# Kernel optimization log

Measured on AMD Instinct MI355X. Metric: run time of the kernel, lower is better.

The kernel has to match this reference:

```python
import jax, jax.numpy as jnp
from jax import lax
import numpy as np

# dims
B, C, H, W, T = 8, 2, 64, 64, 200
# per-layer neuron configs (defaults from NetworkBasic.__init__)
THETA = (30.0, 50.0, 100.0)
TAU_SR = (1.0, 2.0, 4.0)
TAU_REF = (1.0, 2.0, 4.0)
SCALE_REF = (1.0, 1.0, 1.0)
TAU_RHO = (1.0, 1.0, 10.0)


def psp(x, tau):
    """SLAYER synaptic response: first-order leaky integration over time axis (last).
    a[t] = exp(-1/tau) * a[t-1] + x[t]"""
    d = jnp.exp(jnp.asarray(-1.0 / tau, x.dtype))
    xt = jnp.moveaxis(x, -1, 0)  # [T, B, C, H, W]
    def step(a, xi):
        a = d * a + xi
        return a, a
    _, ys = lax.scan(step, jnp.zeros_like(xt[0]), xt)
    return jnp.moveaxis(ys, 0, -1)


def spike(u, theta, tau_ref, scale_ref, tau_rho):
    """SLAYER spiking unit: threshold + leaky refractory state, sequential over T.
    Forward emits hard spikes; surrogate (sigmoid) used only for gradients."""
    dref = jnp.exp(jnp.asarray(-1.0 / tau_ref, u.dtype))
    th = jnp.asarray(theta, u.dtype)
    ut = jnp.moveaxis(u, -1, 0)  # [T, ...]
    def step(r, ui):
        v = ui + r
        hard = (v >= th).astype(u.dtype)
        sur = jax.nn.sigmoid((v - th) / tau_rho)
        s = sur + lax.stop_gradient(hard - sur)  # straight-through surrogate
        r2 = dref * r - th * scale_ref * s       # refractory subtraction
        return r2, s
    _, s = lax.scan(step, jnp.zeros_like(ut[0]), ut)
    return jnp.moveaxis(s, 0, -1)


def conv2d_t(x, w, pad):
    """slayer.conv: spatial conv applied independently per timestep (kernel kxkx1, no bias)."""
    Bb, Cc, Hh, Ww, Tt = x.shape
    xt = jnp.moveaxis(x, -1, 1).reshape(Bb * Tt, Cc, Hh, Ww)
    y = lax.conv_general_dilated(xt, w, (1, 1), [(pad, pad), (pad, pad)],
                                 dimension_numbers=("NCHW", "OIHW", "NCHW"))
    O = w.shape[0]
    return jnp.moveaxis(y.reshape(Bb, Tt, O, Hh, Ww), 1, -1)


def convT2d_t(x, w):
    """slayer.convTranspose kernel=2 stride=2, per timestep (exact 2x upsample)."""
    Bb, Cc, Hh, Ww, Tt = x.shape
    xt = jnp.moveaxis(x, -1, 1).reshape(Bb * Tt, Cc, Hh, Ww)
    y = lax.conv_transpose(xt, w, (2, 2), "VALID",
                           dimension_numbers=("NCHW", "OIHW", "NCHW"))
    O = w.shape[0]
    return jnp.moveaxis(y.reshape(Bb, Tt, O, 2 * Hh, 2 * Ww), 1, -1)


def setup_inputs() -> dict:
    key = jax.random.key(0)
    k0, k1, k2, k3 = jax.random.split(key, 4)
    spikeInput = (jax.random.uniform(k0, (B, C, H, W, T)) < 0.3).astype(jnp.float32)
    w1 = jax.random.normal(k1, (8, 2, 5, 5), jnp.float32) * 10.0
    w2 = jax.random.normal(k2, (8, 8, 3, 3), jnp.float32) * 10.0
    wup = jax.random.normal(k3, (2, 8, 2, 2), jnp.float32) * 10.0
    return {"spikeInput": spikeInput, "w1": w1, "w2": w2, "wup": wup}


def reference(spikeInput, w1, w2, wup):
    Bb, Cc, Hh, Ww, Tt = spikeInput.shape
    psp1 = psp(spikeInput, TAU_SR[0])
    psp1_up = jax.image.resize(psp1, (Bb, Cc, 2 * Hh, 2 * Ww, Tt), method="linear")
    s1 = spike(conv2d_t(psp1, w1, 2), THETA[0], TAU_REF[0], SCALE_REF[0], TAU_RHO[0])
    s2 = spike(conv2d_t(psp(s1, TAU_SR[1]), w2, 1), THETA[1], TAU_REF[1], SCALE_REF[1], TAU_RHO[1])
    s3 = spike(convT2d_t(psp(s2, TAU_SR[2]), wup) + psp1_up,
               THETA[2], TAU_REF[2], SCALE_REF[2], TAU_RHO[2])
    return s3
```

## Files before the change

kernel.cpp:

```cpp
#include <hip/hip_runtime.h>

#define DEC1 0.36787944117144233f
#define DEC2 0.60653065971263342f
#define DEC3 0.77880078307140487f

typedef float v2f __attribute__((ext_vector_type(2)));

__global__ void prep_weights(const float* __restrict__ w1,
                             const float* __restrict__ w2,
                             const float* __restrict__ wup,
                             float* __restrict__ wr)
{
    int i = blockIdx.x * 256 + threadIdx.x;
    if (i < 400) {
        int o = i & 7, tap = i >> 3;
        int c = tap / 25, rem = tap % 25, ky = rem / 5, kx = rem % 5;
        wr[i] = w1[((o * 2 + c) * 5 + ky) * 5 + kx];
    }
    if (i < 576) {
        int o = i & 7, tap = i >> 3;
        int c = tap / 9, rem = tap % 9, ky = rem / 3, kx = rem % 3;
        wr[400 + i] = w2[((o * 8 + c) * 3 + ky) * 3 + kx];
    }
    if (i < 64) {
        int c = i & 7, r = i >> 3;
        int dj = r & 1, di = (r >> 1) & 1, o = r >> 2;
        wr[976 + i] = wup[((o * 8 + c) * 2 + (1 - di)) * 2 + (1 - dj)];
    }
}

static __device__ __forceinline__ float4 spike_psp4(float4 u, float th, float dref,
                                                    float dq, float& r, float& q)
{
    float4 qv; float v, s;
    v = __fadd_rn(u.x, r); s = (v >= th) ? 1.f : 0.f;
    r = __fsub_rn(__fmul_rn(dref, r), __fmul_rn(th, s));
    q = __fadd_rn(__fmul_rn(dq, q), s); qv.x = q;
    v = __fadd_rn(u.y, r); s = (v >= th) ? 1.f : 0.f;
    r = __fsub_rn(__fmul_rn(dref, r), __fmul_rn(th, s));
    q = __fadd_rn(__fmul_rn(dq, q), s); qv.y = q;
    v = __fadd_rn(u.z, r); s = (v >= th) ? 1.f : 0.f;
    r = __fsub_rn(__fmul_rn(dref, r), __fmul_rn(th, s));
    q = __fadd_rn(__fmul_rn(dq, q), s); qv.z = q;
    v = __fadd_rn(u.w, r); s = (v >= th) ? 1.f : 0.f;
    r = __fsub_rn(__fmul_rn(dref, r), __fmul_rn(th, s));
    q = __fadd_rn(__fmul_rn(dq, q), s); qv.w = q;
    return qv;
}

static __device__ __forceinline__ float4 spike4(float4 u, float th, float dref, float& r)
{
    float4 ov; float v, s;
    v = __fadd_rn(u.x, r); s = (v >= th) ? 1.f : 0.f;
    r = __fsub_rn(__fmul_rn(dref, r), __fmul_rn(th, s)); ov.x = s;
    v = __fadd_rn(u.y, r); s = (v >= th) ? 1.f : 0.f;
    r = __fsub_rn(__fmul_rn(dref, r), __fmul_rn(th, s)); ov.y = s;
    v = __fadd_rn(u.z, r); s = (v >= th) ? 1.f : 0.f;
    r = __fsub_rn(__fmul_rn(dref, r), __fmul_rn(th, s)); ov.z = s;
    v = __fadd_rn(u.w, r); s = (v >= th) ? 1.f : 0.f;
    r = __fsub_rn(__fmul_rn(dref, r), __fmul_rn(th, s)); ov.w = s;
    return ov;
}

#define PKFMA(ALO_, AHI_, WV_, DLO_, DHI_) { \
    v2f wv2_ = { (WV_), (WV_) }; \
    ALO_ = __builtin_elementwise_fma(wv2_, DLO_, ALO_); \
    AHI_ = __builtin_elementwise_fma(wv2_, DHI_, AHI_); }

#define PSP4(V_, X_, st) { \
    V_.x = __fadd_rn(__fmul_rn(DEC1, st),   X_.x); \
    V_.y = __fadd_rn(__fmul_rn(DEC1, V_.x), X_.y); \
    V_.z = __fadd_rn(__fmul_rn(DEC1, V_.y), X_.z); \
    V_.w = __fadd_rn(__fmul_rn(DEC1, V_.z), X_.w); st = V_.w; }

__global__ __launch_bounds__(256, 2)
void snn_fused(const float* __restrict__ spk,
               const float* __restrict__ wr,
               float* __restrict__ out)
{
    const int tid  = threadIdx.x;
    const int b    = blockIdx.x >> 6;
    const int tile = blockIdx.x & 63;
    const int gy0  = (tile >> 3) << 3;
    const int gx0  = (tile & 7) << 3;

    __shared__ float4 sP1[2][2][2][224];
    __shared__ float4 sP2[8][2][100];
    __shared__ float4 sP3[8][2][64];

    float aP0 = 0.f, aP1 = 0.f;
    float rB[4], qB[4];
    float rC[2] = {0.f, 0.f}, qC[2] = {0.f, 0.f};
    float r3[2] = {0.f, 0.f};
#pragma unroll
    for (int i = 0; i < 4; ++i) { rB[i] = 0.f; qB[i] = 0.f; }

    const int ary = tid / 14, arx = tid % 14;
    const int aidx = ary * 16 + arx;
    const int aiy = gy0 - 3 + ary, aix = gx0 - 3 + arx;
    const bool avalid = (tid < 196) && (aiy >= 0) && (aiy < 64) && (aix >= 0) && (aix < 64);
    const int aoff0 = avalid ? (((b * 2 + 0) * 64 + aiy) * 64 + aix) * 200 : 0;
    const int aoff1 = avalid ? (((b * 2 + 1) * 64 + aiy) * 64 + aix) * 200 : 0;

    const int bh   = __builtin_amdgcn_readfirstlane(tid >> 7);
    const int bpx  = tid & 127;
    int by_, bx_;
    if (bpx < 80) { by_ = bpx >> 3; bx_ = bpx & 7; }
    else          { int t2 = bpx - 80; by_ = t2 >> 1; bx_ = 8 + (t2 & 1); }
    const int by = by_, bx = bx_;
    const int bwr = by * 10 + bx;
    const int ochB = tid >> 7;

    const int ch2  = __builtin_amdgcn_readfirstlane(tid >> 7);
    const int cop  = __builtin_amdgcn_readfirstlane(tid >> 6) & 1;
    const int cpx  = tid & 63;
    const int cy   = cpx >> 3, cx = cpx & 7;
    const int och2 = (tid >> 6) * 2;

    const int od  = tid >> 7;
    const int ddi = (tid >> 6) & 1;
    const int dpx = tid & 63;
    const int dy  = dpx >> 3, dxx = dpx & 7;
    const int diy = gy0 + dy, dix = gx0 + dxx;

    const float ay  = ddi ? ((diy == 63) ? 1.f : 0.75f) : ((diy == 0) ? 0.f : 0.25f);
    const float byw = ddi ? ((diy == 63) ? 0.f : 0.25f) : ((diy == 0) ? 1.f : 0.75f);
    const float ax0 = (dix == 0)  ? 0.f : 0.25f;
    const float bx0 = (dix == 0)  ? 1.f : 0.75f;
    const float ax1 = (dix == 63) ? 1.f : 0.75f;
    const float bx1 = (dix == 63) ? 0.f : 0.25f;
    const int   didx = (dy + 2 + ddi) * 16 + (dxx + 2);

    float4 x00 = make_float4(0.f,0.f,0.f,0.f), x01 = x00, x10 = x00, x11 = x00;
    if (avalid) {
        x00 = *(const float4*)(spk + aoff0);
        x01 = *(const float4*)(spk + aoff0 + 4);
        x10 = *(const float4*)(spk + aoff1);
        x11 = *(const float4*)(spk + aoff1 + 4);
    }

#pragma unroll 1
    for (int ck = 0; ck < 25; ++ck) {
        const int t0 = ck * 8;
        const int p  = ck & 1;

        if (tid < 196) {
            float4 v;
            PSP4(v, x00, aP0); sP1[p][0][0][aidx] = v;
            PSP4(v, x01, aP0); sP1[p][0][1][aidx] = v;
            PSP4(v, x10, aP1); sP1[p][1][0][aidx] = v;
            PSP4(v, x11, aP1); sP1[p][1][1][aidx] = v;
            if (ck < 24 && avalid) {
                x00 = *(const float4*)(spk + aoff0 + t0 + 8);
                x01 = *(const float4*)(spk + aoff0 + t0 + 12);
                x10 = *(const float4*)(spk + aoff1 + t0 + 8);
                x11 = *(const float4*)(spk + aoff1 + t0 + 12);
            }
        }
        __syncthreads();

        if (bpx < 100) {
            v2f alo[8], ahi[8];
#pragma unroll
            for (int o = 0; o < 8; ++o) { alo[o] = (v2f)(0.f); ahi[o] = (v2f)(0.f); }
#pragma unroll 1
            for (int c = 0; c < 2; ++c) {
#pragma unroll 1
                for (int ky = 0; ky < 5; ++ky) {
                    const float4* r0 = &sP1[p][c][bh][(by + ky) * 16 + bx];
                    const float*  wrow = wr + (c * 25 + ky * 5) * 8;
#pragma unroll
                    for (int kx = 0; kx < 5; ++kx) {
                        float4 d = r0[kx];
                        v2f dlo = { d.x, d.y }, dhi = { d.z, d.w };
#pragma unroll
                        for (int o = 0; o < 8; ++o) {
                            float wv = wrow[kx * 8 + o];
                            PKFMA(alo[o], ahi[o], wv, dlo, dhi);
                        }
                    }
                }
            }
#pragma unroll
            for (int o = 0; o < 8; ++o)
                sP2[o][bh][bwr] = make_float4(alo[o].x, alo[o].y, ahi[o].x, ahi[o].y);
        }
        __syncthreads();

        if (bpx < 100) {
#pragma unroll
            for (int j = 0; j < 4; ++j) {
                const int o = ochB * 4 + j;
                float4 u0 = sP2[o][0][bwr];
                float4 u1 = sP2[o][1][bwr];
                float4 q0 = spike_psp4(u0, 30.f, DEC1, DEC2, rB[j], qB[j]);
                sP2[o][0][bwr] = q0;
                float4 q1 = spike_psp4(u1, 30.f, DEC1, DEC2, rB[j], qB[j]);
                sP2[o][1][bwr] = q1;
            }
        }
        __syncthreads();

        {
            v2f alo[4], ahi[4];
#pragma unroll
            for (int j = 0; j < 4; ++j) { alo[j] = (v2f)(0.f); ahi[j] = (v2f)(0.f); }
            const float* wC = wr + 400 + cop * 4;
#pragma unroll 1
            for (int c = 0; c < 8; ++c) {
#pragma unroll 1
                for (int ky = 0; ky < 3; ++ky) {
                    const float4* r0 = &sP2[c][ch2][(cy + ky) * 10 + cx];
                    const float*  wrow = wC + (c * 9 + ky * 3) * 8;
#pragma unroll
                    for (int kx = 0; kx < 3; ++kx) {
                        float4 d = r0[kx];
                        v2f dlo = { d.x, d.y }, dhi = { d.z, d.w };
#pragma unroll
                        for (int j = 0; j < 4; ++j) {
                            float wv = wrow[kx * 8 + j];
                            PKFMA(alo[j], ahi[j], wv, dlo, dhi);
                        }
                    }
                }
            }
#pragma unroll
            for (int j = 0; j < 4; ++j)
                sP3[cop * 4 + j][ch2][cpx] =
                    make_float4(alo[j].x, alo[j].y, ahi[j].x, ahi[j].y);
        }
        __syncthreads();

        {
#pragma unroll
            for (int j = 0; j < 2; ++j) {
                const int o = och2 + j;
                float4 u0 = sP3[o][0][cpx];
                float4 u1 = sP3[o][1][cpx];
                float4 q0 = spike_psp4(u0, 50.f, DEC2, DEC3, rC[j], qC[j]);
                sP3[o][0][cpx] = q0;
                float4 q1 = spike_psp4(u1, 50.f, DEC2, DEC3, rC[j], qC[j]);
                sP3[o][1][cpx] = q1;
            }
        }
        __syncthreads();

        {
#pragma unroll 1
            for (int h = 0; h < 2; ++h) {
                float4 p3[8];
#pragma unroll
                for (int c = 0; c < 8; ++c) p3[c] = sP3[c][h][dpx];
                float4 P0a = sP1[p][od][h][didx];
                float4 P0b = sP1[p][od][h][didx + 1];
                float4 P0c = sP1[p][od][h][didx + 2];
                float4 P1a = sP1[p][od][h][didx + 16];
                float4 P1b = sP1[p][od][h][didx + 17];
                float4 P1c = sP1[p][od][h][didx + 18];
#pragma unroll
                for (int dj = 0; dj < 2; ++dj) {
                    const float ax  = dj ? ax1 : ax0;
                    const float bxw = dj ? bx1 : bx0;
                    v2f tlo = (v2f)(0.f), thi = (v2f)(0.f);
                    const float* wD = wr + 976 + ((od * 2 + ddi) * 2 + dj) * 8;
#pragma unroll
                    for (int c = 0; c < 8; ++c) {
                        float wv = wD[c];
                        v2f dlo = { p3[c].x, p3[c].y }, dhi = { p3[c].z, p3[c].w };
                        PKFMA(tlo, thi, wv, dlo, dhi);
                    }
                    float4 tv = make_float4(tlo.x, tlo.y, thi.x, thi.y);
                    float4 A  = dj ? P0b : P0a;
                    float4 Bv = dj ? P0c : P0b;
                    float4 Cv = dj ? P1b : P1a;
                    float4 Dv = dj ? P1c : P1b;
                    float4 up, u; float ra, rb;
                    ra = __fadd_rn(__fmul_rn(ay, A.x),  __fmul_rn(byw, Cv.x));
                    rb = __fadd_rn(__fmul_rn(ay, Bv.x), __fmul_rn(byw, Dv.x));
                    up.x = __fadd_rn(__fmul_rn(ax, ra), __fmul_rn(bxw, rb));
                    ra = __fadd_rn(__fmul_rn(ay, A.y),  __fmul_rn(byw, Cv.y));
                    rb = __fadd_rn(__fmul_rn(ay, Bv.y), __fmul_rn(byw, Dv.y));
                    up.y = __fadd_rn(__fmul_rn(ax, ra), __fmul_rn(bxw, rb));
                    ra = __fadd_rn(__fmul_rn(ay, A.z),  __fmul_rn(byw, Cv.z));
                    rb = __fadd_rn(__fmul_rn(ay, Bv.z), __fmul_rn(byw, Dv.z));
                    up.z = __fadd_rn(__fmul_rn(ax, ra), __fmul_rn(bxw, rb));
                    ra = __fadd_rn(__fmul_rn(ay, A.w),  __fmul_rn(byw, Cv.w));
                    rb = __fadd_rn(__fmul_rn(ay, Bv.w), __fmul_rn(byw, Dv.w));
                    up.w = __fadd_rn(__fmul_rn(ax, ra), __fmul_rn(bxw, rb));
                    u.x = __fadd_rn(tv.x, up.x);
                    u.y = __fadd_rn(tv.y, up.y);
                    u.z = __fadd_rn(tv.z, up.z);
                    u.w = __fadd_rn(tv.w, up.w);
                    float4 ov = spike4(u, 100.f, DEC3, r3[dj]);
                    float* op = out + ((((b * 2 + od) * 128 + (2 * diy + ddi)) * 128)
                                       + (2 * dix + dj)) * 200 + t0 + h * 4;
                    *(float4*)op = ov;
                }
            }
        }
    }
}

extern "C" void kernel_launch(void* const* d_in, const int* in_sizes, int n_in,
                              void* d_out, int out_size, void* d_ws, size_t ws_size,
                              hipStream_t stream)
{
    const float* spk = (const float*)d_in[0];
    const float* w1  = (const float*)d_in[1];
    const float* w2  = (const float*)d_in[2];
    const float* wup = (const float*)d_in[3];
    float* outp = (float*)d_out;
    float* wr   = (float*)d_ws;

    prep_weights<<<dim3(3), dim3(256), 0, stream>>>(w1, w2, wup, wr);
    snn_fused<<<dim3(512), dim3(256), 0, stream>>>(spk, wr, outp);
}
```

Before: 569.6 us.

## Split block into producer/consumer halves pipelining layer-1 and layers 2-3 across chunks

The block is split into two 128-thread halves. The first half computes input PSP, conv1 and the layer-1 spike for chunk ck, while the second half runs conv2, the layer-2 spike, the transposed conv and the output spike for chunk ck-1. This cuts barriers per chunk from five to two and overlaps the two stage groups. In exchange each half does more work per thread, register pressure rises from more accumulators, and the loop gains one extra iteration to drain the pipeline.

```diff
diff --git a/kernel.cpp b/kernel.cpp
--- a/kernel.cpp
+++ b/kernel.cpp
@@ -88,89 +88,115 @@
     __shared__ float4 sP2[8][2][100];
     __shared__ float4 sP3[8][2][64];
 
-    float aP0 = 0.f, aP1 = 0.f;
-    float rB[4], qB[4];
-    float rC[2] = {0.f, 0.f}, qC[2] = {0.f, 0.f};
-    float r3[2] = {0.f, 0.f};
-#pragma unroll
-    for (int i = 0; i < 4; ++i) { rB[i] = 0.f; qB[i] = 0.f; }
-
-    const int ary = tid / 14, arx = tid % 14;
-    const int aidx = ary * 16 + arx;
-    const int aiy = gy0 - 3 + ary, aix = gx0 - 3 + arx;
-    const bool avalid = (tid < 196) && (aiy >= 0) && (aiy < 64) && (aix >= 0) && (aix < 64);
-    const int aoff0 = avalid ? (((b * 2 + 0) * 64 + aiy) * 64 + aix) * 200 : 0;
-    const int aoff1 = avalid ? (((b * 2 + 1) * 64 + aiy) * 64 + aix) * 200 : 0;
-
-    const int bh   = __builtin_amdgcn_readfirstlane(tid >> 7);
-    const int bpx  = tid & 127;
-    int by_, bx_;
-    if (bpx < 80) { by_ = bpx >> 3; bx_ = bpx & 7; }
-    else          { int t2 = bpx - 80; by_ = t2 >> 1; bx_ = 8 + (t2 & 1); }
-    const int by = by_, bx = bx_;
-    const int bwr = by * 10 + bx;
-    const int ochB = tid >> 7;
-
-    const int ch2  = __builtin_amdgcn_readfirstlane(tid >> 7);
-    const int cop  = __builtin_amdgcn_readfirstlane(tid >> 6) & 1;
-    const int cpx  = tid & 63;
-    const int cy   = cpx >> 3, cx = cpx & 7;
-    const int och2 = (tid >> 6) * 2;
-
-    const int od  = tid >> 7;
-    const int ddi = (tid >> 6) & 1;
-    const int dpx = tid & 63;
-    const int dy  = dpx >> 3, dxx = dpx & 7;
-    const int diy = gy0 + dy, dix = gx0 + dxx;
-
-    const float ay  = ddi ? ((diy == 63) ? 1.f : 0.75f) : ((diy == 0) ? 0.f : 0.25f);
-    const float byw = ddi ? ((diy == 63) ? 0.f : 0.25f) : ((diy == 0) ? 1.f : 0.75f);
-    const float ax0 = (dix == 0)  ? 0.f : 0.25f;
-    const float bx0 = (dix == 0)  ? 1.f : 0.75f;
-    const float ax1 = (dix == 63) ? 1.f : 0.75f;
-    const float bx1 = (dix == 63) ? 0.f : 0.25f;
-    const int   didx = (dy + 2 + ddi) * 16 + (dxx + 2);
+    const bool isP = tid < 128;
+
+    const bool u1ok = isP && ((tid + 128) < 196);
+    int aidx0 = 0, aoff00 = 0, aoff01 = 0; bool av0 = false;
+    int aidx1 = 0, aoff10 = 0, aoff11 = 0; bool av1 = false;
+    if (isP) {
+        int ry = tid / 14, rx = tid % 14;
+        aidx0 = ry * 16 + rx;
+        int iy = gy0 - 3 + ry, ix = gx0 - 3 + rx;
+        av0 = iy >= 0 && iy < 64 && ix >= 0 && ix < 64;
+        if (av0) { aoff00 = (((b*2+0)*64 + iy)*64 + ix)*200;
+                   aoff01 = (((b*2+1)*64 + iy)*64 + ix)*200; }
+        if (u1ok) {
+            int u = tid + 128; ry = u / 14; rx = u % 14;
+            aidx1 = ry * 16 + rx;
+            iy = gy0 - 3 + ry; ix = gx0 - 3 + rx;
+            av1 = iy >= 0 && iy < 64 && ix >= 0 && ix < 64;
+            if (av1) { aoff10 = (((b*2+0)*64 + iy)*64 + ix)*200;
+                       aoff11 = (((b*2+1)*64 + iy)*64 + ix)*200; }
+        }
+    }
+    float aP00 = 0.f, aP01 = 0.f, aP10 = 0.f, aP11 = 0.f;
+
+    int by = 0, bx = 0, bwr = 0;
+    { int bpx = tid;
+      if (bpx < 80) { by = bpx >> 3; bx = bpx & 7; }
+      else          { int t2 = bpx - 80; by = t2 >> 1; bx = 8 + (t2 & 1); }
+      bwr = by * 10 + bx; }
+    float rB[8], qB[8];
+#pragma unroll
+    for (int i = 0; i < 8; ++i) { rB[i] = 0.f; qB[i] = 0.f; }
+
+    const int qt  = tid & 127;
+    const int wq  = qt >> 6;
+    const int l   = qt & 63;
+    const int pxq = wq * 32 + (l & 31);
+    const int sel = l >> 5;
+    const int cy  = pxq >> 3, cx = pxq & 7;
+    const int diy = gy0 + cy, dix = gx0 + cx;
+    float rC[4], qC[4];
+#pragma unroll
+    for (int i = 0; i < 4; ++i) { rC[i] = 0.f; qC[i] = 0.f; }
+    float r3[2][2] = {{0.f, 0.f}, {0.f, 0.f}};
+    const float ay0  = (diy == 0)  ? 0.f : 0.25f, by0w = (diy == 0)  ? 1.f : 0.75f;
+    const float ay1  = (diy == 63) ? 1.f : 0.75f, by1w = (diy == 63) ? 0.f : 0.25f;
+    const float ax0  = (dix == 0)  ? 0.f : 0.25f, bx0w = (dix == 0)  ? 1.f : 0.75f;
+    const float ax1  = (dix == 63) ? 1.f : 0.75f, bx1w = (dix == 63) ? 0.f : 0.25f;
+    const int   didx0 = (cy + 2) * 16 + (cx + 2);
 
     float4 x00 = make_float4(0.f,0.f,0.f,0.f), x01 = x00, x10 = x00, x11 = x00;
-    if (avalid) {
-        x00 = *(const float4*)(spk + aoff0);
-        x01 = *(const float4*)(spk + aoff0 + 4);
-        x10 = *(const float4*)(spk + aoff1);
-        x11 = *(const float4*)(spk + aoff1 + 4);
-    }
-
-#pragma unroll 1
-    for (int ck = 0; ck < 25; ++ck) {
-        const int t0 = ck * 8;
-        const int p  = ck & 1;
-
-        if (tid < 196) {
-            float4 v;
-            PSP4(v, x00, aP0); sP1[p][0][0][aidx] = v;
-            PSP4(v, x01, aP0); sP1[p][0][1][aidx] = v;
-            PSP4(v, x10, aP1); sP1[p][1][0][aidx] = v;
-            PSP4(v, x11, aP1); sP1[p][1][1][aidx] = v;
-            if (ck < 24 && avalid) {
-                x00 = *(const float4*)(spk + aoff0 + t0 + 8);
-                x01 = *(const float4*)(spk + aoff0 + t0 + 12);
-                x10 = *(const float4*)(spk + aoff1 + t0 + 8);
-                x11 = *(const float4*)(spk + aoff1 + t0 + 12);
-            }
-        }
-        __syncthreads();
-
-        if (bpx < 100) {
+    float4 y00 = x00, y01 = x00, y10 = x00, y11 = x00;
+    if (av0) {
+        x00 = *(const float4*)(spk + aoff00);
+        x01 = *(const float4*)(spk + aoff00 + 4);
+        x10 = *(const float4*)(spk + aoff01);
+        x11 = *(const float4*)(spk + aoff01 + 4);
+    }
+    if (av1) {
+        y00 = *(const float4*)(spk + aoff10);
+        y01 = *(const float4*)(spk + aoff10 + 4);
+        y10 = *(const float4*)(spk + aoff11);
+        y11 = *(const float4*)(spk + aoff11 + 4);
+    }
+
+#pragma unroll 1
+    for (int ck = 0; ck < 26; ++ck) {
+        const int p = ck & 1;
+
+        if (isP) {
+            if (ck < 25) {
+                const int t0 = ck * 8;
+                float4 v;
+                PSP4(v, x00, aP00); sP1[p][0][0][aidx0] = v;
+                PSP4(v, x01, aP00); sP1[p][0][1][aidx0] = v;
+                PSP4(v, x10, aP01); sP1[p][1][0][aidx0] = v;
+                PSP4(v, x11, aP01); sP1[p][1][1][aidx0] = v;
+                if (u1ok) {
+                    PSP4(v, y00, aP10); sP1[p][0][0][aidx1] = v;
+                    PSP4(v, y01, aP10); sP1[p][0][1][aidx1] = v;
+                    PSP4(v, y10, aP11); sP1[p][1][0][aidx1] = v;
+                    PSP4(v, y11, aP11); sP1[p][1][1][aidx1] = v;
+                }
+                if (ck < 24) {
+                    if (av0) {
+                        x00 = *(const float4*)(spk + aoff00 + t0 + 8);
+                        x01 = *(const float4*)(spk + aoff00 + t0 + 12);
+                        x10 = *(const float4*)(spk + aoff01 + t0 + 8);
+                        x11 = *(const float4*)(spk + aoff01 + t0 + 12);
+                    }
+                    if (av1) {
+                        y00 = *(const float4*)(spk + aoff10 + t0 + 8);
+                        y01 = *(const float4*)(spk + aoff10 + t0 + 12);
+                        y10 = *(const float4*)(spk + aoff11 + t0 + 8);
+                        y11 = *(const float4*)(spk + aoff11 + t0 + 12);
+                    }
+                }
+            }
+        } else if (ck >= 1) {
             v2f alo[8], ahi[8];
 #pragma unroll
             for (int o = 0; o < 8; ++o) { alo[o] = (v2f)(0.f); ahi[o] = (v2f)(0.f); }
 #pragma unroll 1
-            for (int c = 0; c < 2; ++c) {
-#pragma unroll 1
-                for (int ky = 0; ky < 5; ++ky) {
-                    const float4* r0 = &sP1[p][c][bh][(by + ky) * 16 + bx];
-                    const float*  wrow = wr + (c * 25 + ky * 5) * 8;
-#pragma unroll
-                    for (int kx = 0; kx < 5; ++kx) {
+            for (int c = 0; c < 8; ++c) {
+#pragma unroll 1
+                for (int ky = 0; ky < 3; ++ky) {
+                    const float4* r0 = &sP2[c][sel][(cy + ky) * 10 + cx];
+                    const float*  wrow = wr + 400 + (c * 9 + ky * 3) * 8;
+#pragma unroll
+                    for (int kx = 0; kx < 3; ++kx) {
                         float4 d = r0[kx];
                         v2f dlo = { d.x, d.y }, dhi = { d.z, d.w };
 #pragma unroll
@@ -183,121 +209,125 @@
             }
 #pragma unroll
             for (int o = 0; o < 8; ++o)
-                sP2[o][bh][bwr] = make_float4(alo[o].x, alo[o].y, ahi[o].x, ahi[o].y);
+                sP3[o][sel][pxq] = make_float4(alo[o].x, alo[o].y, ahi[o].x, ahi[o].y);
         }
         __syncthreads();
 
-        if (bpx < 100) {
+        if (isP) {
+            if (ck < 25 && tid < 100) {
+                v2f a0lo[8], a0hi[8], a1lo[8], a1hi[8];
+#pragma unroll
+                for (int o = 0; o < 8; ++o) {
+                    a0lo[o] = (v2f)(0.f); a0hi[o] = (v2f)(0.f);
+                    a1lo[o] = (v2f)(0.f); a1hi[o] = (v2f)(0.f);
+                }
+#pragma unroll 1
+                for (int c = 0; c < 2; ++c) {
+#pragma unroll 1
+                    for (int ky = 0; ky < 5; ++ky) {
+                        const float4* r0 = &sP1[p][c][0][(by + ky) * 16 + bx];
+                        const float4* r1 = &sP1[p][c][1][(by + ky) * 16 + bx];
+                        const float*  wrow = wr + (c * 25 + ky * 5) * 8;
+#pragma unroll
+                        for (int kx = 0; kx < 5; ++kx) {
+                            float4 d0 = r0[kx], d1 = r1[kx];
+                            v2f d0lo = { d0.x, d0.y }, d0hi = { d0.z, d0.w };
+                            v2f d1lo = { d1.x, d1.y }, d1hi = { d1.z, d1.w };
+#pragma unroll
+                            for (int o = 0; o < 8; ++o) {
+                                float wv = wrow[kx * 8 + o];
+                                PKFMA(a0lo[o], a0hi[o], wv, d0lo, d0hi);
+                                PKFMA(a1lo[o], a1hi[o], wv, d1lo, d1hi);
+                            }
+                        }
+                    }
+                }
+#pragma unroll
+                for (int o = 0; o < 8; ++o) {
+                    float4 u0 = make_float4(a0lo[o].x, a0lo[o].y, a0hi[o].x, a0hi[o].y);
+                    float4 q0 = spike_psp4(u0, 30.f, DEC1, DEC2, rB[o], qB[o]);
+                    sP2[o][0][bwr] = q0;
+                    float4 u1 = make_float4(a1lo[o].x, a1lo[o].y, a1hi[o].x, a1hi[o].y);
+                    float4 q1 = spike_psp4(u1, 30.f, DEC1, DEC2, rB[o], qB[o]);
+                    sP2[o][1][bwr] = q1;
+                }
+            }
+        } else if (ck >= 1) {
+            const int pD  = (ck - 1) & 1;
+            const int t0m = (ck - 1) * 8;
 #pragma unroll
             for (int j = 0; j < 4; ++j) {
-                const int o = ochB * 4 + j;
-                float4 u0 = sP2[o][0][bwr];
-                float4 u1 = sP2[o][1][bwr];
-                float4 q0 = spike_psp4(u0, 30.f, DEC1, DEC2, rB[j], qB[j]);
-                sP2[o][0][bwr] = q0;
-                float4 q1 = spike_psp4(u1, 30.f, DEC1, DEC2, rB[j], qB[j]);
-                sP2[o][1][bwr] = q1;
+                const int o = sel * 4 + j;
+                float4 u0 = sP3[o][0][pxq];
+                float4 u1 = sP3[o][1][pxq];
+                float4 q0 = spike_psp4(u0, 50.f, DEC2, DEC3, rC[j], qC[j]);
+                sP3[o][0][pxq] = q0;
+                float4 q1 = spike_psp4(u1, 50.f, DEC2, DEC3, rC[j], qC[j]);
+                sP3[o][1][pxq] = q1;
+            }
+            float4 p30[8], p31[8];
+#pragma unroll
+            for (int c2 = 0; c2 < 8; ++c2) {
+                p30[c2] = sP3[c2][0][pxq];
+                p31[c2] = sP3[c2][1][pxq];
+            }
+#pragma unroll
+            for (int h = 0; h < 2; ++h) {
+#pragma unroll
+                for (int ddi = 0; ddi < 2; ++ddi) {
+                    const float ayv = ddi ? ay1 : ay0;
+                    const float byv = ddi ? by1w : by0w;
+                    const int base = didx0 + ddi * 16;
+                    float4 Pa = sP1[pD][sel][h][base];
+                    float4 Pb = sP1[pD][sel][h][base + 1];
+                    float4 Pc = sP1[pD][sel][h][base + 2];
+                    float4 Qa = sP1[pD][sel][h][base + 16];
+                    float4 Qb = sP1[pD][sel][h][base + 17];
+                    float4 Qc = sP1[pD][sel][h][base + 18];
+#pragma unroll
+                    for (int dj = 0; dj < 2; ++dj) {
+                        const float axv = dj ? ax1 : ax0;
+                        const float bxv = dj ? bx1w : bx0w;
+                        v2f tlo = (v2f)(0.f), thi = (v2f)(0.f);
+                        const float* wD = wr + 976 + ((sel * 2 + ddi) * 2 + dj) * 8;
+#pragma unroll
+                        for (int c2 = 0; c2 < 8; ++c2) {
+                            float wv = wD[c2];
+                            float4 pc = h ? p31[c2] : p30[c2];
+                            v2f dlo = { pc.x, pc.y }, dhi = { pc.z, pc.w };
+                            PKFMA(tlo, thi, wv, dlo, dhi);
+                        }
+                        float4 tv = make_float4(tlo.x, tlo.y, thi.x, thi.y);
+                        float4 A  = dj ? Pb : Pa;
+                        float4 Bv = dj ? Pc : Pb;
+                        float4 Cv = dj ? Qb : Qa;
+                        float4 Dv = dj ? Qc : Qb;
+                        float4 up, u; float ra, rb;
+                        ra = __fadd_rn(__fmul_rn(ayv, A.x),  __fmul_rn(byv, Cv.x));
+                        rb = __fadd_rn(__fmul_rn(ayv, Bv.x), __fmul_rn(byv, Dv.x));
+                        up.x = __fadd_rn(__fmul_rn(axv, ra), __fmul_rn(bxv, rb));
+                        ra = __fadd_rn(__fmul_rn(ayv, A.y),  __fmul_rn(byv, Cv.y));
+                        rb = __fadd_rn(__fmul_rn(ayv, Bv.y), __fmul_rn(byv, Dv.y));
+                        up.y = __fadd_rn(__fmul_rn(axv, ra), __fmul_rn(bxv, rb));
+                        ra = __fadd_rn(__fmul_rn(ayv, A.z),  __fmul_rn(byv, Cv.z));
+                        rb = __fadd_rn(__fmul_rn(ayv, Bv.z), __fmul_rn(byv, Dv.z));
+                        up.z = __fadd_rn(__fmul_rn(axv, ra), __fmul_rn(bxv, rb));
+                        ra = __fadd_rn(__fmul_rn(ayv, A.w),  __fmul_rn(byv, Cv.w));
+                        rb = __fadd_rn(__fmul_rn(ayv, Bv.w), __fmul_rn(byv, Dv.w));
+                        up.w = __fadd_rn(__fmul_rn(axv, ra), __fmul_rn(bxv, rb));
+                        u.x = __fadd_rn(tv.x, up.x);
+                        u.y = __fadd_rn(tv.y, up.y);
+                        u.z = __fadd_rn(tv.z, up.z);
+                        u.w = __fadd_rn(tv.w, up.w);
+                        float4 ov = spike4(u, 100.f, DEC3, r3[ddi][dj]);
+                        float* op = out + ((((b * 2 + sel) * 128 + (2 * diy + ddi)) * 128)
+                                           + (2 * dix + dj)) * 200 + t0m + h * 4;
+                        *(float4*)op = ov;
+                    }
+                }
             }
         }
         __syncthreads();
-
-        {
-            v2f alo[4], ahi[4];
-#pragma unroll
-            for (int j = 0; j < 4; ++j) { alo[j] = (v2f)(0.f); ahi[j] = (v2f)(0.f); }
-            const float* wC = wr + 400 + cop * 4;
-#pragma unroll 1
-            for (int c = 0; c < 8; ++c) {
-#pragma unroll 1
-                for (int ky = 0; ky < 3; ++ky) {
-                    const float4* r0 = &sP2[c][ch2][(cy + ky) * 10 + cx];
-                    const float*  wrow = wC + (c * 9 + ky * 3) * 8;
-#pragma unroll
-                    for (int kx = 0; kx < 3; ++kx) {
-                        float4 d = r0[kx];
-                        v2f dlo = { d.x, d.y }, dhi = { d.z, d.w };
-#pragma unroll
-                        for (int j = 0; j < 4; ++j) {
-                            float wv = wrow[kx * 8 + j];
-                            PKFMA(alo[j], ahi[j], wv, dlo, dhi);
-                        }
-                    }
-                }
-            }
-#pragma unroll
-            for (int j = 0; j < 4; ++j)
-                sP3[cop * 4 + j][ch2][cpx] =
-                    make_float4(alo[j].x, alo[j].y, ahi[j].x, ahi[j].y);
-        }
-        __syncthreads();
-
-        {
-#pragma unroll
-            for (int j = 0; j < 2; ++j) {
-                const int o = och2 + j;
-                float4 u0 = sP3[o][0][cpx];
-                float4 u1 = sP3[o][1][cpx];
-                float4 q0 = spike_psp4(u0, 50.f, DEC2, DEC3, rC[j], qC[j]);
-                sP3[o][0][cpx] = q0;
-                float4 q1 = spike_psp4(u1, 50.f, DEC2, DEC3, rC[j], qC[j]);
-                sP3[o][1][cpx] = q1;
-            }
-        }
-        __syncthreads();
-
-        {
-#pragma unroll 1
-            for (int h = 0; h < 2; ++h) {
-                float4 p3[8];
-#pragma unroll
-                for (int c = 0; c < 8; ++c) p3[c] = sP3[c][h][dpx];
-                float4 P0a = sP1[p][od][h][didx];
-                float4 P0b = sP1[p][od][h][didx + 1];
-                float4 P0c = sP1[p][od][h][didx + 2];
-                float4 P1a = sP1[p][od][h][didx + 16];
-                float4 P1b = sP1[p][od][h][didx + 17];
-                float4 P1c = sP1[p][od][h][didx + 18];
-#pragma unroll
-                for (int dj = 0; dj < 2; ++dj) {
-                    const float ax  = dj ? ax1 : ax0;
-                    const float bxw = dj ? bx1 : bx0;
-                    v2f tlo = (v2f)(0.f), thi = (v2f)(0.f);
-                    const float* wD = wr + 976 + ((od * 2 + ddi) * 2 + dj) * 8;
-#pragma unroll
-                    for (int c = 0; c < 8; ++c) {
-                        float wv = wD[c];
-                        v2f dlo = { p3[c].x, p3[c].y }, dhi = { p3[c].z, p3[c].w };
-                        PKFMA(tlo, thi, wv, dlo, dhi);
-                    }
-                    float4 tv = make_float4(tlo.x, tlo.y, thi.x, thi.y);
-                    float4 A  = dj ? P0b : P0a;
-                    float4 Bv = dj ? P0c : P0b;
-                    float4 Cv = dj ? P1b : P1a;
-                    float4 Dv = dj ? P1c : P1b;
-                    float4 up, u; float ra, rb;
-                    ra = __fadd_rn(__fmul_rn(ay, A.x),  __fmul_rn(byw, Cv.x));
-                    rb = __fadd_rn(__fmul_rn(ay, Bv.x), __fmul_rn(byw, Dv.x));
-                    up.x = __fadd_rn(__fmul_rn(ax, ra), __fmul_rn(bxw, rb));
-                    ra = __fadd_rn(__fmul_rn(ay, A.y),  __fmul_rn(byw, Cv.y));
-                    rb = __fadd_rn(__fmul_rn(ay, Bv.y), __fmul_rn(byw, Dv.y));
-                    up.y = __fadd_rn(__fmul_rn(ax, ra), __fmul_rn(bxw, rb));
-                    ra = __fadd_rn(__fmul_rn(ay, A.z),  __fmul_rn(byw, Cv.z));
-                    rb = __fadd_rn(__fmul_rn(ay, Bv.z), __fmul_rn(byw, Dv.z));
-                    up.z = __fadd_rn(__fmul_rn(ax, ra), __fmul_rn(bxw, rb));
-                    ra = __fadd_rn(__fmul_rn(ay, A.w),  __fmul_rn(byw, Cv.w));
-                    rb = __fadd_rn(__fmul_rn(ay, Bv.w), __fmul_rn(byw, Dv.w));
-                    up.w = __fadd_rn(__fmul_rn(ax, ra), __fmul_rn(bxw, rb));
-                    u.x = __fadd_rn(tv.x, up.x);
-                    u.y = __fadd_rn(tv.y, up.y);
-                    u.z = __fadd_rn(tv.z, up.z);
-                    u.w = __fadd_rn(tv.w, up.w);
-                    float4 ov = spike4(u, 100.f, DEC3, r3[dj]);
-                    float* op = out + ((((b * 2 + od) * 128 + (2 * diy + ddi)) * 128)
-                                       + (2 * dix + dj)) * 200 + t0 + h * 4;
-                    *(float4*)op = ov;
-                }
-            }
-        }
     }
 }
 
```

Result: slower. 636.2 us (+11.7%).
